# Kernel optimization log

Measured on AMD Instinct MI355X. Metric: run time of the kernel, lower is better.

The kernel has to match this reference:

```python
import jax, jax.numpy as jnp
import numpy as np

B, N = 128, 128
FEAT_IN = 6   # feature_dim(4) + class + score
E = 32        # embedding_dim
NUM_CLASSES = 80


def setup_inputs() -> dict:
    key = jax.random.key(0)
    ks = jax.random.split(key, 20)
    def glorot(k, shape):
        fan_in, fan_out = shape[0], shape[1]
        lim = jnp.sqrt(6.0 / (fan_in + fan_out)).astype(jnp.float32)
        return jax.random.uniform(k, shape, jnp.float32, -lim, lim)
    return {
        'boxes': jax.random.uniform(ks[0], (B, N, 4), jnp.float32),
        'classes': jax.random.randint(ks[1], (B, N), 0, NUM_CLASSES),
        'scores': jax.random.uniform(ks[2], (B, N), jnp.float32),
        'num_objects': jax.random.randint(ks[3], (B,), 1, N + 1),
        # feature_encoder: Linear(6->32), ReLU, Linear(32->32)
        'W1': glorot(ks[4], (FEAT_IN, E)), 'b1': jnp.zeros((E,), jnp.float32),
        'W2': glorot(ks[5], (E, E)),       'b2': jnp.zeros((E,), jnp.float32),
        # isObject: Linear(32->32), ReLU, Linear(32->1), Sigmoid
        'Wo1': glorot(ks[6], (E, E)),  'bo1': jnp.zeros((E,), jnp.float32),
        'Wo2': glorot(ks[7], (E, 1)),  'bo2': jnp.zeros((1,), jnp.float32),
        # sameClass: Linear(64->32), ReLU, Linear(32->1), Sigmoid
        'Ws1': glorot(ks[8], (2 * E, E)), 'bs1': jnp.zeros((E,), jnp.float32),
        'Ws2': glorot(ks[9], (E, 1)),     'bs2': jnp.zeros((1,), jnp.float32),
    }


def reference(boxes, classes, scores, num_objects, W1, b1, W2, b2,
              Wo1, bo1, Wo2, bo2, Ws1, bs1, Ws2, bs2):
    # encode: [B,N,6] -> [B,N,E]
    combined = jnp.concatenate(
        [boxes, classes.astype(jnp.float32)[..., None], scores[..., None]], axis=-1)
    enc = jax.nn.relu(combined @ W1 + b1) @ W2 + b2                 # [B,N,E]

    # isObject predicate -> [B,N]
    isobj = jax.nn.sigmoid(jax.nn.relu(enc @ Wo1 + bo1) @ Wo2 + bo2)[..., 0]

    # sameClass on all pairs: split concat-weight so we never build [B,N,N,2E]
    Wsx, Wsy = Ws1[:E], Ws1[E:]
    hx = enc @ Wsx                                                  # [B,N,E]
    hy = enc @ Wsy                                                  # [B,N,E]
    h = jax.nn.relu(hx[:, :, None, :] + hy[:, None, :, :] + bs1)    # [B,N,N,E]
    same = jax.nn.sigmoid(h @ Ws2 + bs2)[..., 0]                    # [B,N,N] (x,y)

    # inner = And_min(isObject(y), sameClass(x,y))
    inner = jnp.minimum(isobj[:, None, :], same)                    # [B,N,N]

    mask = jnp.arange(N)[None, :] < num_objects[:, None]            # [B,N] valid objs
    n = num_objects.astype(jnp.float32)
    denom = jnp.maximum(n, 1.0)

    # Exists_y = mean over valid y
    exists = jnp.sum(inner * mask[:, None, :], axis=-1) / denom[:, None]  # [B,N]

    # outer = Or_max(Not(isObject(x)), exists)
    outer = jnp.maximum(1.0 - isobj, exists)                        # [B,N]

    # Forall_x = min over valid x (pad with 1.0, never the min for valid batches)
    sat_b = jnp.min(jnp.where(mask, outer, 1.0), axis=-1)           # [B]

    valid = (num_objects > 0).astype(jnp.float32)
    cnt = jnp.sum(valid)
    total = jnp.where(cnt > 0,
                      jnp.sum(sat_b * valid) / jnp.maximum(cnt, 1.0),
                      jnp.float32(1.0))
    return total
```

## Files before the change

### kernel.cpp

```cpp
#include <hip/hip_runtime.h>

#define BB 128
#define NN 128
#define EE 32

#define HX_OFF  0
#define HY_OFF  (16384 * 32)
#define ISO_OFF (2 * 16384 * 32)
#define SAT_OFF (ISO_OFF + 16384)
#define CNT_OFF (SAT_OFF + 128)

__global__ __launch_bounds__(256) void encode_kernel(
    const float* __restrict__ boxes, const int* __restrict__ classes,
    const float* __restrict__ scores,
    const float* __restrict__ W1, const float* __restrict__ b1,
    const float* __restrict__ W2, const float* __restrict__ b2,
    const float* __restrict__ Wo1, const float* __restrict__ bo1,
    const float* __restrict__ Wo2, const float* __restrict__ bo2,
    const float* __restrict__ Ws1, float* __restrict__ ws)
{
    const int t = threadIdx.x;

    if (blockIdx.x == 0) {
        if (t < 128) ((int*)ws)[SAT_OFF + t] = 0x3F800000;
        if (t == 128) ((int*)ws)[CNT_OFF] = 0;
    }

    const int item = blockIdx.x * 8 + (t >> 5);
    const int e = t & 31;

    const float* bx = boxes + item * 4;
    const float c0 = bx[0];
    const float c1 = bx[1];
    const float c2 = bx[2];
    const float c3 = bx[3];
    const float c4 = (float)classes[item];
    const float c5 = scores[item];

    float h1 = b1[e];
    h1 = fmaf(c0, W1[0 * 32 + e], h1);
    h1 = fmaf(c1, W1[1 * 32 + e], h1);
    h1 = fmaf(c2, W1[2 * 32 + e], h1);
    h1 = fmaf(c3, W1[3 * 32 + e], h1);
    h1 = fmaf(c4, W1[4 * 32 + e], h1);
    h1 = fmaf(c5, W1[5 * 32 + e], h1);
    h1 = fmaxf(h1, 0.f);

    float enc = b2[e];
#pragma unroll
    for (int k = 0; k < 32; k++) {
        enc = fmaf(__shfl(h1, k, 32), W2[k * 32 + e], enc);
    }

    float u = bo1[e];
    float hx = 0.f, hy = 0.f;
#pragma unroll
    for (int k = 0; k < 32; k++) {
        const float ek = __shfl(enc, k, 32);
        u  = fmaf(ek, Wo1[k * 32 + e], u);
        hx = fmaf(ek, Ws1[k * 32 + e], hx);
        hy = fmaf(ek, Ws1[(32 + k) * 32 + e], hy);
    }
    u = fmaxf(u, 0.f);

    float v = u * Wo2[e];
#pragma unroll
    for (int off = 16; off >= 1; off >>= 1) v += __shfl_xor(v, off, 32);

    ws[HX_OFF + item * 32 + e] = hx;
    ws[HY_OFF + item * 32 + e] = hy;
    if (e == 0) {
        const float z = v + bo2[0];
        ws[ISO_OFF + item] = 1.f / (1.f + __expf(-z));
    }
}

__global__ __launch_bounds__(256) void pairs_kernel(
    const float* __restrict__ bs1, const float* __restrict__ Ws2,
    const float* __restrict__ bs2, const int* __restrict__ num_objects,
    float* __restrict__ ws, float* __restrict__ out, int nblocks)
{
    __shared__ float hyS[128 * 36];
    __shared__ float isoS[128];
    __shared__ float wred[4];
    __shared__ int lastFlag;
    __shared__ float r1[4], r2[4];

    const int t = threadIdx.x;
    const int b = blockIdx.x >> 2;
    const int q = blockIdx.x & 3;

    const float* hyg = ws + HY_OFF + b * 128 * 32;
#pragma unroll
    for (int it = 0; it < 16; it++) {
        const int idx = t + it * 256;
        hyS[(idx >> 5) * 36 + (idx & 31)] = hyg[idx];
    }
    if (t < 128) isoS[t] = ws[ISO_OFF + b * 128 + t];
    __syncthreads();

    const int nb = num_objects[b];
    const int i = q * 32 + (t >> 3);
    const int s = t & 7;

    float hxb[32];
    const float* hxg = ws + HX_OFF + (b * 128 + i) * 32;
#pragma unroll
    for (int k = 0; k < 32; k++) hxb[k] = hxg[k] + bs1[k];
    float w2[32];
#pragma unroll
    for (int k = 0; k < 32; k++) w2[k] = Ws2[k];
    const float bb = bs2[0];

    float acc = 0.f;
    for (int j = s; j < nb; j += 8) {
        const float* hr = hyS + j * 36;
        float d = bb;
#pragma unroll
        for (int k = 0; k < 32; k++) {
            d = fmaf(fmaxf(hxb[k] + hr[k], 0.f), w2[k], d);
        }
        const float same = 1.f / (1.f + __expf(-d));
        acc += fminf(isoS[j], same);
    }
    acc += __shfl_xor(acc, 1);
    acc += __shfl_xor(acc, 2);
    acc += __shfl_xor(acc, 4);

    const float exists = acc / (float)(nb > 1 ? nb : 1);
    const float outer = fmaxf(1.f - isoS[i], exists);
    float val = (i < nb) ? outer : 1.f;

    val = fminf(val, __shfl_xor(val, 8));
    val = fminf(val, __shfl_xor(val, 16));
    val = fminf(val, __shfl_xor(val, 32));
    if ((t & 63) == 0) wred[t >> 6] = val;
    __syncthreads();

    if (t == 0) {
        const float m = fminf(fminf(wred[0], wred[1]), fminf(wred[2], wred[3]));
        atomicMin((int*)ws + SAT_OFF + b, __float_as_int(m));
        __threadfence();
        const int old = __hip_atomic_fetch_add((int*)ws + CNT_OFF, 1,
                                               __ATOMIC_ACQ_REL, __HIP_MEMORY_SCOPE_AGENT);
        lastFlag = (old == nblocks - 1) ? 1 : 0;
    }
    __syncthreads();

    if (lastFlag) {
        float contrib = 0.f, vcnt = 0.f;
        if (t < 128) {
            const int nbt = num_objects[t];
            const int sbits = __hip_atomic_load((int*)ws + SAT_OFF + t,
                                                __ATOMIC_RELAXED, __HIP_MEMORY_SCOPE_AGENT);
            const float sat = __int_as_float(sbits);
            const float valid = (nbt > 0) ? 1.f : 0.f;
            contrib = sat * valid;
            vcnt = valid;
        }
#pragma unroll
        for (int off = 1; off < 64; off <<= 1) {
            contrib += __shfl_xor(contrib, off);
            vcnt += __shfl_xor(vcnt, off);
        }
        if ((t & 63) == 0) { r1[t >> 6] = contrib; r2[t >> 6] = vcnt; }
        __syncthreads();
        if (t == 0) {
            const float sc = r1[0] + r1[1] + r1[2] + r1[3];
            const float cn = r2[0] + r2[1] + r2[2] + r2[3];
            out[0] = (cn > 0.f) ? (sc / cn) : 1.f;
        }
    }
}

extern "C" void kernel_launch(void* const* d_in, const int* in_sizes, int n_in,
                              void* d_out, int out_size, void* d_ws, size_t ws_size,
                              hipStream_t stream)
{
    const float* boxes       = (const float*)d_in[0];
    const int*   classes     = (const int*)d_in[1];
    const float* scores      = (const float*)d_in[2];
    const int*   num_objects = (const int*)d_in[3];
    const float* W1  = (const float*)d_in[4];
    const float* b1  = (const float*)d_in[5];
    const float* W2  = (const float*)d_in[6];
    const float* b2  = (const float*)d_in[7];
    const float* Wo1 = (const float*)d_in[8];
    const float* bo1 = (const float*)d_in[9];
    const float* Wo2 = (const float*)d_in[10];
    const float* bo2 = (const float*)d_in[11];
    const float* Ws1 = (const float*)d_in[12];
    const float* bs1 = (const float*)d_in[13];
    const float* Ws2 = (const float*)d_in[14];
    const float* bs2 = (const float*)d_in[15];

    float* ws  = (float*)d_ws;
    float* out = (float*)d_out;

    encode_kernel<<<2048, 256, 0, stream>>>(boxes, classes, scores,
                                            W1, b1, W2, b2, Wo1, bo1, Wo2, bo2,
                                            Ws1, ws);
    const int nblocks = 128 * 4;
    pairs_kernel<<<nblocks, 256, 0, stream>>>(bs1, Ws2, bs2, num_objects,
                                              ws, out, nblocks);
}
```

Measured before the change: 112.7 us.

## Fuse encoder into pairs kernel, recomputing per-batch encodings in shared memory

Removes the separate encode kernel: each pairs block now computes the encoder MLP for all 128 objects of its batch and writes hy, isObject and its own 32 hx rows directly into shared memory, avoiding the global round-trip through the workspace. The workspace init moves to a hipMemsetAsync using 0x7F7F7F7F as both the atomicMin seed and the counter base. The inner pair loop reads hy rows as float4. The trade-off is that each batch's encoding is computed redundantly four times, and the memset is a separate operation on the stream.

```diff
diff --git a/kernel.cpp b/kernel.cpp
--- a/kernel.cpp
+++ b/kernel.cpp
@@ -4,84 +4,22 @@
 #define NN 128
 #define EE 32
 
-#define HX_OFF  0
-#define HY_OFF  (16384 * 32)
-#define ISO_OFF (2 * 16384 * 32)
-#define SAT_OFF (ISO_OFF + 16384)
-#define CNT_OFF (SAT_OFF + 128)
+#define CNT_BASE 0x7F7F7F7Fu
 
-__global__ __launch_bounds__(256) void encode_kernel(
+__global__ __launch_bounds__(256, 2) void ltn_fused(
     const float* __restrict__ boxes, const int* __restrict__ classes,
-    const float* __restrict__ scores,
+    const float* __restrict__ scores, const int* __restrict__ num_objects,
     const float* __restrict__ W1, const float* __restrict__ b1,
     const float* __restrict__ W2, const float* __restrict__ b2,
     const float* __restrict__ Wo1, const float* __restrict__ bo1,
     const float* __restrict__ Wo2, const float* __restrict__ bo2,
-    const float* __restrict__ Ws1, float* __restrict__ ws)
-{
-    const int t = threadIdx.x;
-
-    if (blockIdx.x == 0) {
-        if (t < 128) ((int*)ws)[SAT_OFF + t] = 0x3F800000;
-        if (t == 128) ((int*)ws)[CNT_OFF] = 0;
-    }
-
-    const int item = blockIdx.x * 8 + (t >> 5);
-    const int e = t & 31;
-
-    const float* bx = boxes + item * 4;
-    const float c0 = bx[0];
-    const float c1 = bx[1];
-    const float c2 = bx[2];
-    const float c3 = bx[3];
-    const float c4 = (float)classes[item];
-    const float c5 = scores[item];
-
-    float h1 = b1[e];
-    h1 = fmaf(c0, W1[0 * 32 + e], h1);
-    h1 = fmaf(c1, W1[1 * 32 + e], h1);
-    h1 = fmaf(c2, W1[2 * 32 + e], h1);
-    h1 = fmaf(c3, W1[3 * 32 + e], h1);
-    h1 = fmaf(c4, W1[4 * 32 + e], h1);
-    h1 = fmaf(c5, W1[5 * 32 + e], h1);
-    h1 = fmaxf(h1, 0.f);
-
-    float enc = b2[e];
-#pragma unroll
-    for (int k = 0; k < 32; k++) {
-        enc = fmaf(__shfl(h1, k, 32), W2[k * 32 + e], enc);
-    }
-
-    float u = bo1[e];
-    float hx = 0.f, hy = 0.f;
-#pragma unroll
-    for (int k = 0; k < 32; k++) {
-        const float ek = __shfl(enc, k, 32);
-        u  = fmaf(ek, Wo1[k * 32 + e], u);
-        hx = fmaf(ek, Ws1[k * 32 + e], hx);
-        hy = fmaf(ek, Ws1[(32 + k) * 32 + e], hy);
-    }
-    u = fmaxf(u, 0.f);
-
-    float v = u * Wo2[e];
-#pragma unroll
-    for (int off = 16; off >= 1; off >>= 1) v += __shfl_xor(v, off, 32);
-
-    ws[HX_OFF + item * 32 + e] = hx;
-    ws[HY_OFF + item * 32 + e] = hy;
-    if (e == 0) {
-        const float z = v + bo2[0];
-        ws[ISO_OFF + item] = 1.f / (1.f + __expf(-z));
-    }
-}
-
-__global__ __launch_bounds__(256) void pairs_kernel(
-    const float* __restrict__ bs1, const float* __restrict__ Ws2,
-    const float* __restrict__ bs2, const int* __restrict__ num_objects,
-    float* __restrict__ ws, float* __restrict__ out, int nblocks)
+    const float* __restrict__ Ws1, const float* __restrict__ bs1,
+    const float* __restrict__ Ws2, const float* __restrict__ bs2,
+    unsigned* __restrict__ ws, float* __restrict__ out, int nblocks)
 {
     __shared__ float hyS[128 * 36];
     __shared__ float isoS[128];
+    __shared__ float hxS[32 * 33];
     __shared__ float wred[4];
     __shared__ int lastFlag;
     __shared__ float r1[4], r2[4];
@@ -90,35 +28,79 @@
     const int b = blockIdx.x >> 2;
     const int q = blockIdx.x & 3;
 
-    const float* hyg = ws + HY_OFF + b * 128 * 32;
+#pragma unroll 1
+    for (int pass = 0; pass < 16; ++pass) {
+        const int il = pass * 8 + (t >> 5);
+        const int e  = t & 31;
+        const int item = b * 128 + il;
+
+        const float* bx = boxes + item * 4;
+        const float c0 = bx[0];
+        const float c1 = bx[1];
+        const float c2 = bx[2];
+        const float c3 = bx[3];
+        const float c4 = (float)classes[item];
+        const float c5 = scores[item];
+
+        float h1 = b1[e];
+        h1 = fmaf(c0, W1[0 * 32 + e], h1);
+        h1 = fmaf(c1, W1[1 * 32 + e], h1);
+        h1 = fmaf(c2, W1[2 * 32 + e], h1);
+        h1 = fmaf(c3, W1[3 * 32 + e], h1);
+        h1 = fmaf(c4, W1[4 * 32 + e], h1);
+        h1 = fmaf(c5, W1[5 * 32 + e], h1);
+        h1 = fmaxf(h1, 0.f);
+
+        float enc = b2[e];
 #pragma unroll
-    for (int it = 0; it < 16; it++) {
-        const int idx = t + it * 256;
-        hyS[(idx >> 5) * 36 + (idx & 31)] = hyg[idx];
+        for (int k = 0; k < 32; k++)
+            enc = fmaf(__shfl(h1, k, 32), W2[k * 32 + e], enc);
+
+        float u = bo1[e];
+        float hx = 0.f, hy = 0.f;
+#pragma unroll
+        for (int k = 0; k < 32; k++) {
+            const float ek = __shfl(enc, k, 32);
+            u  = fmaf(ek, Wo1[k * 32 + e], u);
+            hx = fmaf(ek, Ws1[k * 32 + e], hx);
+            hy = fmaf(ek, Ws1[(32 + k) * 32 + e], hy);
+        }
+        u = fmaxf(u, 0.f);
+
+        float v = u * Wo2[e];
+#pragma unroll
+        for (int off = 16; off >= 1; off >>= 1) v += __shfl_xor(v, off, 32);
+
+        hyS[il * 36 + e] = hy;
+        if ((il >> 5) == q) hxS[(il & 31) * 33 + e] = hx;
+        if (e == 0) isoS[il] = 1.f / (1.f + __expf(-(v + bo2[0])));
     }
-    if (t < 128) isoS[t] = ws[ISO_OFF + b * 128 + t];
     __syncthreads();
 
     const int nb = num_objects[b];
-    const int i = q * 32 + (t >> 3);
-    const int s = t & 7;
+    const int il = t >> 3;
+    const int i  = q * 32 + il;
+    const int s  = t & 7;
 
     float hxb[32];
-    const float* hxg = ws + HX_OFF + (b * 128 + i) * 32;
 #pragma unroll
-    for (int k = 0; k < 32; k++) hxb[k] = hxg[k] + bs1[k];
+    for (int k = 0; k < 32; k++) hxb[k] = hxS[il * 33 + k] + bs1[k];
     float w2[32];
 #pragma unroll
     for (int k = 0; k < 32; k++) w2[k] = Ws2[k];
-    const float bb = bs2[0];
+    const float bbias = bs2[0];
 
     float acc = 0.f;
     for (int j = s; j < nb; j += 8) {
-        const float* hr = hyS + j * 36;
-        float d = bb;
+        const float4* hr4 = (const float4*)(hyS + j * 36);
+        float d = bbias;
 #pragma unroll
-        for (int k = 0; k < 32; k++) {
-            d = fmaf(fmaxf(hxb[k] + hr[k], 0.f), w2[k], d);
+        for (int kk = 0; kk < 8; kk++) {
+            const float4 h = hr4[kk];
+            d = fmaf(fmaxf(hxb[4 * kk + 0] + h.x, 0.f), w2[4 * kk + 0], d);
+            d = fmaf(fmaxf(hxb[4 * kk + 1] + h.y, 0.f), w2[4 * kk + 1], d);
+            d = fmaf(fmaxf(hxb[4 * kk + 2] + h.z, 0.f), w2[4 * kk + 2], d);
+            d = fmaf(fmaxf(hxb[4 * kk + 3] + h.w, 0.f), w2[4 * kk + 3], d);
         }
         const float same = 1.f / (1.f + __expf(-d));
         acc += fminf(isoS[j], same);
@@ -139,11 +121,11 @@
 
     if (t == 0) {
         const float m = fminf(fminf(wred[0], wred[1]), fminf(wred[2], wred[3]));
-        atomicMin((int*)ws + SAT_OFF + b, __float_as_int(m));
+        atomicMin(ws + b, __float_as_uint(m));
         __threadfence();
-        const int old = __hip_atomic_fetch_add((int*)ws + CNT_OFF, 1,
-                                               __ATOMIC_ACQ_REL, __HIP_MEMORY_SCOPE_AGENT);
-        lastFlag = (old == nblocks - 1) ? 1 : 0;
+        const unsigned old = __hip_atomic_fetch_add(ws + 128, 1u,
+                                                    __ATOMIC_ACQ_REL, __HIP_MEMORY_SCOPE_AGENT);
+        lastFlag = ((old - CNT_BASE) == (unsigned)(nblocks - 1)) ? 1 : 0;
     }
     __syncthreads();
 
@@ -151,9 +133,9 @@
         float contrib = 0.f, vcnt = 0.f;
         if (t < 128) {
             const int nbt = num_objects[t];
-            const int sbits = __hip_atomic_load((int*)ws + SAT_OFF + t,
-                                                __ATOMIC_RELAXED, __HIP_MEMORY_SCOPE_AGENT);
-            const float sat = __int_as_float(sbits);
+            const unsigned sbits = __hip_atomic_load(ws + t, __ATOMIC_RELAXED,
+                                                     __HIP_MEMORY_SCOPE_AGENT);
+            const float sat = __uint_as_float(sbits);
             const float valid = (nbt > 0) ? 1.f : 0.f;
             contrib = sat * valid;
             vcnt = valid;
@@ -194,13 +176,13 @@
     const float* Ws2 = (const float*)d_in[14];
     const float* bs2 = (const float*)d_in[15];
 
-    float* ws  = (float*)d_ws;
-    float* out = (float*)d_out;
+    unsigned* ws  = (unsigned*)d_ws;
+    float*    out = (float*)d_out;
 
-    encode_kernel<<<2048, 256, 0, stream>>>(boxes, classes, scores,
-                                            W1, b1, W2, b2, Wo1, bo1, Wo2, bo2,
-                                            Ws1, ws);
+    hipMemsetAsync(ws, 0x7F, 129 * sizeof(unsigned), stream);
+
     const int nblocks = 128 * 4;
-    pairs_kernel<<<nblocks, 256, 0, stream>>>(bs1, Ws2, bs2, num_objects,
-                                              ws, out, nblocks);
+    ltn_fused<<<nblocks, 256, 0, stream>>>(boxes, classes, scores, num_objects,
+                                           W1, b1, W2, b2, Wo1, bo1, Wo2, bo2,
+                                           Ws1, bs1, Ws2, bs2, ws, out, nblocks);
 }
```

Measured after the change: 130.5 us. 15.8% more time.

## Stage encoder weights in LDS, vectorize loads, split FMA chains, memset init

Applied to the files above, without the earlier changes.

The encoder kernel now copies all MLP weights into shared memory and exchanges activations through an LDS row read as float4 instead of per-element warp shuffles. The pairs kernel loads hy with float4 and splits the 32-term dot product into four independent accumulators to shorten the dependency chain. Initialization of the per-batch min slots and the block counter moves from the encoder kernel to a hipMemsetAsync with a 0x7F pattern, with unsigned atomics and a counter base offset to match. This adds a third stream operation and per-block weight-staging overhead in the encoder.

```diff
diff --git a/kernel.cpp b/kernel.cpp
--- a/kernel.cpp
+++ b/kernel.cpp
@@ -4,11 +4,12 @@
 #define NN 128
 #define EE 32
 
-#define HX_OFF  0
-#define HY_OFF  (16384 * 32)
-#define ISO_OFF (2 * 16384 * 32)
-#define SAT_OFF (ISO_OFF + 16384)
-#define CNT_OFF (SAT_OFF + 128)
+#define SAT_OFF 0
+#define CNT_OFF 128
+#define HX_OFF  256
+#define HY_OFF  (HX_OFF + 16384 * 32)
+#define ISO_OFF (HY_OFF + 16384 * 32)
+#define CNT_BASE 0x7F7F7F7Fu
 
 __global__ __launch_bounds__(256) void encode_kernel(
     const float* __restrict__ boxes, const int* __restrict__ classes,
@@ -19,60 +20,88 @@
     const float* __restrict__ Wo2, const float* __restrict__ bo2,
     const float* __restrict__ Ws1, float* __restrict__ ws)
 {
+    __shared__ float sm[4740];
+
     const int t = threadIdx.x;
 
-    if (blockIdx.x == 0) {
-        if (t < 128) ((int*)ws)[SAT_OFF + t] = 0x3F800000;
-        if (t == 128) ((int*)ws)[CNT_OFF] = 0;
-    }
-
-    const int item = blockIdx.x * 8 + (t >> 5);
-    const int e = t & 31;
-
-    const float* bx = boxes + item * 4;
-    const float c0 = bx[0];
-    const float c1 = bx[1];
-    const float c2 = bx[2];
-    const float c3 = bx[3];
+    ((float4*)(sm + 224))[t]        = ((const float4*)W2)[t];
+    ((float4*)(sm + 1280))[t]       = ((const float4*)Wo1)[t];
+    ((float4*)(sm + 2692))[t]       = ((const float4*)Ws1)[t];
+    ((float4*)(sm + 2692))[t + 256] = ((const float4*)Ws1)[t + 256];
+    if (t < 48) ((float4*)sm)[t] = ((const float4*)W1)[t];
+    if (t < 32) {
+        sm[192 + t]  = b1[t];
+        sm[1248 + t] = b2[t];
+        sm[2304 + t] = bo1[t];
+        sm[2336 + t] = Wo2[t];
+    }
+    if (t == 0) sm[2368] = bo2[0];
+    __syncthreads();
+
+    const int il = t >> 5;
+    const int e  = t & 31;
+    const int item = blockIdx.x * 8 + il;
+
+    const float4 bx = ((const float4*)boxes)[item];
     const float c4 = (float)classes[item];
     const float c5 = scores[item];
 
-    float h1 = b1[e];
-    h1 = fmaf(c0, W1[0 * 32 + e], h1);
-    h1 = fmaf(c1, W1[1 * 32 + e], h1);
-    h1 = fmaf(c2, W1[2 * 32 + e], h1);
-    h1 = fmaf(c3, W1[3 * 32 + e], h1);
-    h1 = fmaf(c4, W1[4 * 32 + e], h1);
-    h1 = fmaf(c5, W1[5 * 32 + e], h1);
+    float h1 = sm[192 + e];
+    h1 = fmaf(bx.x, sm[0 * 32 + e], h1);
+    h1 = fmaf(bx.y, sm[1 * 32 + e], h1);
+    h1 = fmaf(bx.z, sm[2 * 32 + e], h1);
+    h1 = fmaf(bx.w, sm[3 * 32 + e], h1);
+    h1 = fmaf(c4,   sm[4 * 32 + e], h1);
+    h1 = fmaf(c5,   sm[5 * 32 + e], h1);
     h1 = fmaxf(h1, 0.f);
 
-    float enc = b2[e];
-#pragma unroll
-    for (int k = 0; k < 32; k++) {
-        enc = fmaf(__shfl(h1, k, 32), W2[k * 32 + e], enc);
-    }
-
-    float u = bo1[e];
+    float* row = sm + 2372 + il * 40;
+    row[e] = h1;
+
+    float a0 = 0.f, a1 = 0.f, a2 = 0.f, a3 = 0.f;
+#pragma unroll
+    for (int kk = 0; kk < 8; kk++) {
+        const float4 h = *(const float4*)(row + kk * 4);
+        a0 = fmaf(h.x, sm[224 + (4 * kk + 0) * 32 + e], a0);
+        a1 = fmaf(h.y, sm[224 + (4 * kk + 1) * 32 + e], a1);
+        a2 = fmaf(h.z, sm[224 + (4 * kk + 2) * 32 + e], a2);
+        a3 = fmaf(h.w, sm[224 + (4 * kk + 3) * 32 + e], a3);
+    }
+    const float enc = ((a0 + a1) + (a2 + a3)) + sm[1248 + e];
+    row[e] = enc;
+
+    float u = sm[2304 + e];
     float hx = 0.f, hy = 0.f;
 #pragma unroll
-    for (int k = 0; k < 32; k++) {
-        const float ek = __shfl(enc, k, 32);
-        u  = fmaf(ek, Wo1[k * 32 + e], u);
-        hx = fmaf(ek, Ws1[k * 32 + e], hx);
-        hy = fmaf(ek, Ws1[(32 + k) * 32 + e], hy);
+    for (int kk = 0; kk < 8; kk++) {
+        const float4 ec = *(const float4*)(row + kk * 4);
+        const int k0 = 4 * kk;
+        u  = fmaf(ec.x, sm[1280 + (k0 + 0) * 32 + e], u);
+        u  = fmaf(ec.y, sm[1280 + (k0 + 1) * 32 + e], u);
+        u  = fmaf(ec.z, sm[1280 + (k0 + 2) * 32 + e], u);
+        u  = fmaf(ec.w, sm[1280 + (k0 + 3) * 32 + e], u);
+        hx = fmaf(ec.x, sm[2692 + (k0 + 0) * 32 + e], hx);
+        hx = fmaf(ec.y, sm[2692 + (k0 + 1) * 32 + e], hx);
+        hx = fmaf(ec.z, sm[2692 + (k0 + 2) * 32 + e], hx);
+        hx = fmaf(ec.w, sm[2692 + (k0 + 3) * 32 + e], hx);
+        hy = fmaf(ec.x, sm[2692 + (32 + k0 + 0) * 32 + e], hy);
+        hy = fmaf(ec.y, sm[2692 + (32 + k0 + 1) * 32 + e], hy);
+        hy = fmaf(ec.z, sm[2692 + (32 + k0 + 2) * 32 + e], hy);
+        hy = fmaf(ec.w, sm[2692 + (32 + k0 + 3) * 32 + e], hy);
     }
     u = fmaxf(u, 0.f);
 
-    float v = u * Wo2[e];
-#pragma unroll
-    for (int off = 16; off >= 1; off >>= 1) v += __shfl_xor(v, off, 32);
+    float v = u * sm[2336 + e];
+    v += __shfl_xor(v, 16, 32);
+    v += __shfl_xor(v, 8, 32);
+    v += __shfl_xor(v, 4, 32);
+    v += __shfl_xor(v, 2, 32);
+    v += __shfl_xor(v, 1, 32);
 
     ws[HX_OFF + item * 32 + e] = hx;
     ws[HY_OFF + item * 32 + e] = hy;
-    if (e == 0) {
-        const float z = v + bo2[0];
-        ws[ISO_OFF + item] = 1.f / (1.f + __expf(-z));
-    }
+    if (e == 0)
+        ws[ISO_OFF + item] = 1.f / (1.f + __expf(-(v + sm[2368])));
 }
 
 __global__ __launch_bounds__(256) void pairs_kernel(
@@ -90,11 +119,11 @@
     const int b = blockIdx.x >> 2;
     const int q = blockIdx.x & 3;
 
-    const float* hyg = ws + HY_OFF + b * 128 * 32;
-#pragma unroll
-    for (int it = 0; it < 16; it++) {
+    const float4* hyg4 = (const float4*)(ws + HY_OFF + b * 128 * 32);
+#pragma unroll
+    for (int it = 0; it < 4; it++) {
         const int idx = t + it * 256;
-        hyS[(idx >> 5) * 36 + (idx & 31)] = hyg[idx];
+        ((float4*)(hyS + (idx >> 3) * 36))[idx & 7] = hyg4[idx];
     }
     if (t < 128) isoS[t] = ws[ISO_OFF + b * 128 + t];
     __syncthreads();
@@ -110,16 +139,22 @@
     float w2[32];
 #pragma unroll
     for (int k = 0; k < 32; k++) w2[k] = Ws2[k];
-    const float bb = bs2[0];
+    const float bbias = bs2[0];
 
     float acc = 0.f;
     for (int j = s; j < nb; j += 8) {
-        const float* hr = hyS + j * 36;
-        float d = bb;
-#pragma unroll
-        for (int k = 0; k < 32; k++) {
-            d = fmaf(fmaxf(hxb[k] + hr[k], 0.f), w2[k], d);
-        }
+        const float4* hr4 = (const float4*)(hyS + j * 36);
+        float d0 = bbias, d1 = 0.f, d2 = 0.f, d3 = 0.f;
+#pragma unroll
+        for (int kk = 0; kk < 8; kk++) {
+            const float4 h = hr4[kk];
+            const int k0 = 4 * kk;
+            d0 = fmaf(fmaxf(hxb[k0 + 0] + h.x, 0.f), w2[k0 + 0], d0);
+            d1 = fmaf(fmaxf(hxb[k0 + 1] + h.y, 0.f), w2[k0 + 1], d1);
+            d2 = fmaf(fmaxf(hxb[k0 + 2] + h.z, 0.f), w2[k0 + 2], d2);
+            d3 = fmaf(fmaxf(hxb[k0 + 3] + h.w, 0.f), w2[k0 + 3], d3);
+        }
+        const float d = (d0 + d1) + (d2 + d3);
         const float same = 1.f / (1.f + __expf(-d));
         acc += fminf(isoS[j], same);
     }
@@ -139,11 +174,11 @@
 
     if (t == 0) {
         const float m = fminf(fminf(wred[0], wred[1]), fminf(wred[2], wred[3]));
-        atomicMin((int*)ws + SAT_OFF + b, __float_as_int(m));
+        atomicMin((unsigned*)ws + SAT_OFF + b, __float_as_uint(m));
         __threadfence();
-        const int old = __hip_atomic_fetch_add((int*)ws + CNT_OFF, 1,
-                                               __ATOMIC_ACQ_REL, __HIP_MEMORY_SCOPE_AGENT);
-        lastFlag = (old == nblocks - 1) ? 1 : 0;
+        const unsigned old = __hip_atomic_fetch_add((unsigned*)ws + CNT_OFF, 1u,
+                                                    __ATOMIC_ACQ_REL, __HIP_MEMORY_SCOPE_AGENT);
+        lastFlag = ((old - CNT_BASE) == (unsigned)(nblocks - 1)) ? 1 : 0;
     }
     __syncthreads();
 
@@ -151,9 +186,9 @@
         float contrib = 0.f, vcnt = 0.f;
         if (t < 128) {
             const int nbt = num_objects[t];
-            const int sbits = __hip_atomic_load((int*)ws + SAT_OFF + t,
-                                                __ATOMIC_RELAXED, __HIP_MEMORY_SCOPE_AGENT);
-            const float sat = __int_as_float(sbits);
+            const unsigned sbits = __hip_atomic_load((unsigned*)ws + SAT_OFF + t,
+                                                     __ATOMIC_RELAXED, __HIP_MEMORY_SCOPE_AGENT);
+            const float sat = __uint_as_float(sbits);
             const float valid = (nbt > 0) ? 1.f : 0.f;
             contrib = sat * valid;
             vcnt = valid;
@@ -197,6 +232,8 @@
     float* ws  = (float*)d_ws;
     float* out = (float*)d_out;
 
+    hipMemsetAsync(ws, 0x7F, 129 * sizeof(float), stream);
+
     encode_kernel<<<2048, 256, 0, stream>>>(boxes, classes, scores,
                                             W1, b1, W2, b2, Wo1, bo1, Wo2, bo2,
                                             Ws1, ws);
```

Result: no change. 113.8 us (+1.0%).
